# Optimization experiments

Measured on AMD Instinct MI355X. Metric: run time of the kernel, lower is better.

The kernel has to match this reference:

```python
import jax, jax.numpy as jnp
import numpy as np

B, C, T, V = 16, 128, 64, 512
H = 8
AC = C // H  # att_channel = 16
NEG = -1e9


def setup_inputs() -> dict:
    key = jax.random.key(0)
    ks = jax.random.split(key, 6)
    x = jax.random.normal(ks[0], (B, C, T, V), dtype=jnp.float32)
    # additive temporal mask: causal (upper triangle masked out)
    mask = jnp.where(jnp.triu(jnp.ones((T, T), dtype=bool), k=1), NEG, 0.0).astype(jnp.float32)
    # to_qkv: nn.Linear(att_channel -> 3*att_channel); torch weight is [out, in]
    w_qkv = jax.random.normal(ks[1], (3 * AC, AC), dtype=jnp.float32) / np.sqrt(AC)
    b_qkv = jax.random.normal(ks[2], (3 * AC,), dtype=jnp.float32) * 0.02
    # proj: Linear(n_channel -> n_channel)
    w_proj = jax.random.normal(ks[3], (C, C), dtype=jnp.float32) / np.sqrt(C)
    b_proj = jax.random.normal(ks[4], (C,), dtype=jnp.float32) * 0.02
    return {"x": x, "mask": mask, "w_qkv": w_qkv, "b_qkv": b_qkv,
            "w_proj": w_proj, "b_proj": b_proj}


def reference(x, mask, w_qkv, b_qkv, w_proj, b_proj):
    # split_head: 'b (h c) t v -> (b h) v t c'
    xh = x.reshape(B, H, AC, T, V)
    xh = jnp.transpose(xh, (0, 1, 4, 3, 2)).reshape(B * H, V, T, AC)
    # to_qkv on last dim
    qkv = jnp.einsum('nvtc,oc->nvto', xh, w_qkv) + b_qkv
    q, k, v = qkv[..., :AC], qkv[..., AC:2 * AC], qkv[..., 2 * AC:]
    # attention over time, batched over (b h, v)
    att = jnp.einsum('nvtc,nvsc->nvts', q, k) / jnp.sqrt(jnp.float32(AC)) + mask
    att = jax.nn.softmax(att, axis=-1)
    out = jnp.einsum('nvts,nvsc->nvtc', att, v)  # [(b h), v, t, c]
    # concat_head: '(b h) v t c -> b (h c) t v'
    out = out.reshape(B, H, V, T, AC)
    out = jnp.transpose(out, (0, 1, 4, 3, 2)).reshape(B, C, T, V)
    # proj: bctv -> bvtc, Linear(C->C), back
    y = jnp.einsum('bctv,oc->botv', out, w_proj) + b_proj[None, :, None, None]
    return y
```

## Files before the change

### kernel.cpp

```cpp
#include <hip/hip_runtime.h>
#include <math.h>

#define B_ 16
#define C_ 128
#define T_ 64
#define V_ 512
#define H_ 8

typedef short shortx8 __attribute__((ext_vector_type(8)));
typedef float floatx16 __attribute__((ext_vector_type(16)));

static __device__ __forceinline__ unsigned int f2bf(float f) {
  unsigned int u = __float_as_uint(f);
  return (u + 0x7FFFu + ((u >> 16) & 1u)) >> 16;
}


__global__ __launch_bounds__(256) void precompute_kernel(
    const float* __restrict__ w_qkv,
    const float* __restrict__ b_qkv,
    const float* __restrict__ w_proj,
    const float* __restrict__ b_proj,
    float* __restrict__ ws) {
  const float SC = 0.25f * 1.4426950408889634f;
  int tid = threadIdx.x;

  {
    int c = tid >> 4, cp = tid & 15;
    float s = 0.f;
    for (int a = 0; a < 16; ++a)
      s += w_qkv[a * 16 + c] * w_qkv[(16 + a) * 16 + cp];
    ws[c * 16 + cp] = s * SC;
  }
  if (tid < 16) {
    float s = 0.f;
    for (int a = 0; a < 16; ++a)
      s += b_qkv[a] * w_qkv[(16 + a) * 16 + tid];
    ws[256 + tid] = s * SC;
  }
  if (tid < 128) {
    float s = b_proj[tid];
    for (int a = 0; a < 16; ++a) {
      float wpsum = 0.f;
      for (int h = 0; h < 8; ++h) wpsum += w_proj[tid * 128 + h * 16 + a];
      s += wpsum * b_qkv[32 + a];
    }
    ws[272 + tid] = s;
  }
  unsigned short* gf = (unsigned short*)(ws + 512);
  for (int k = 0; k < 64; ++k) {
    int idx = tid + 256 * k;
    int o = idx >> 7;
    int hc = idx & 127;
    int h = hc >> 4, c = hc & 15;
    float s = 0.f;
    for (int a = 0; a < 16; ++a)
      s += w_proj[o * 128 + h * 16 + a] * w_qkv[(32 + a) * 16 + c];
    int w = o >> 5, lm = o & 31;
    int kk = hc >> 4;
    int half = (hc >> 3) & 1;
    int j = hc & 7;
    int lane = half * 32 + lm;
    gf[((w * 8 + kk) * 64 + lane) * 8 + j] = (unsigned short)f2bf(s);
  }
}

__global__ __launch_bounds__(256, 2) void attn_kernel(
    const float* __restrict__ x,
    const float* __restrict__ ws,
    float* __restrict__ out) {
  __shared__ float Xs[16][64][16];

  int blk = blockIdx.x;
  int vt = blk & 31;
  int h  = (blk >> 5) & 7;
  int b  = blk >> 8;
  int v0 = vt * 16;
  int tid = threadIdx.x;

  const float* xb = x + ((size_t)(b * C_ + h * 16) * T_) * V_ + v0;
  #pragma unroll
  for (int k = 0; k < 16; ++k) {
    int i4 = tid + 256 * k;
    int vq = (i4 & 3) * 4;
    int s  = (i4 >> 2) & 63;
    int c  = i4 >> 8;
    *(float4*)&Xs[c][s][vq] = *(const float4*)(xb + ((size_t)c * 64 + s) * 512 + vq);
  }
  __syncthreads();

  const float* M = ws;
  const float* u = ws + 256;
  int vl = tid & 15;
  int tq = tid >> 4;
  int t0 = tq * 4;

  float q2[4][16];
  #pragma unroll
  for (int cp = 0; cp < 16; ++cp) {
    float uv = u[cp];
    q2[0][cp] = uv; q2[1][cp] = uv; q2[2][cp] = uv; q2[3][cp] = uv;
  }
  #pragma unroll
  for (int c = 0; c < 16; ++c) {
    float x0 = Xs[c][t0 + 0][vl];
    float x1 = Xs[c][t0 + 1][vl];
    float x2 = Xs[c][t0 + 2][vl];
    float x3 = Xs[c][t0 + 3][vl];
    #pragma unroll
    for (int cp = 0; cp < 16; ++cp) {
      float m = M[c * 16 + cp];
      q2[0][cp] += x0 * m; q2[1][cp] += x1 * m;
      q2[2][cp] += x2 * m; q2[3][cp] += x3 * m;
    }
  }

  float z[4][16];
  #pragma unroll
  for (int tt = 0; tt < 4; ++tt)
    #pragma unroll
    for (int c = 0; c < 16; ++c) z[tt][c] = 0.f;
  float sum0 = 0.f, sum1 = 0.f, sum2 = 0.f, sum3 = 0.f;

  for (int s = 0; s <= t0 + 3; ++s) {
    float xr[16];
    #pragma unroll
    for (int c = 0; c < 16; ++c) xr[c] = Xs[c][s][vl];
    float d0 = 0.f, d1 = 0.f, d2 = 0.f, d3 = 0.f;
    #pragma unroll
    for (int c = 0; c < 16; ++c) {
      d0 += q2[0][c] * xr[c];
      d1 += q2[1][c] * xr[c];
      d2 += q2[2][c] * xr[c];
      d3 += q2[3][c] * xr[c];
    }
    float e0 = (s <= t0 + 0) ? __builtin_amdgcn_exp2f(d0) : 0.f;
    float e1 = (s <= t0 + 1) ? __builtin_amdgcn_exp2f(d1) : 0.f;
    float e2 = (s <= t0 + 2) ? __builtin_amdgcn_exp2f(d2) : 0.f;
    float e3 = __builtin_amdgcn_exp2f(d3);
    sum0 += e0; sum1 += e1; sum2 += e2; sum3 += e3;
    #pragma unroll
    for (int c = 0; c < 16; ++c) {
      z[0][c] += e0 * xr[c];
      z[1][c] += e1 * xr[c];
      z[2][c] += e2 * xr[c];
      z[3][c] += e3 * xr[c];
    }
  }

  float rsum[4] = {1.f / sum0, 1.f / sum1, 1.f / sum2, 1.f / sum3};

  #pragma unroll
  for (int tt = 0; tt < 4; ++tt) {
    float rs = rsum[tt];
    int t = t0 + tt;
    size_t PB = (size_t)b * (C_ * T_ * V_) + (size_t)t * V_ + (size_t)(vt >> 2) * 64;
    #pragma unroll
    for (int half = 0; half < 2; ++half) {
      int hcblk = 2 * h + half;
      uint4 pk;
      unsigned int* pw = (unsigned int*)&pk;
      #pragma unroll
      for (int wq = 0; wq < 4; ++wq) {
        int c = half * 8 + wq * 2;
        pw[wq] = f2bf(z[tt][c] * rs) | (f2bf(z[tt][c + 1] * rs) << 16);
      }
      float* dst = out + PB + (size_t)(hcblk * 4 + (vt & 3)) * (T_ * V_) + vl * 4;
      *(uint4*)dst = pk;
    }
  }
}

__global__ __launch_bounds__(256) void proj_kernel(
    const float* __restrict__ ws,
    float* __restrict__ out) {
  int blk = blockIdx.x;
  int vt = blk & 7;
  int t  = (blk >> 3) & 63;
  int b  = blk >> 9;
  int v0 = vt * 64;
  int tid = threadIdx.x;
  int l  = tid & 63;
  int w  = tid >> 6;
  int lh = l >> 5;
  int lm = l & 31;

  size_t PB = (size_t)b * (C_ * T_ * V_) + (size_t)t * V_ + v0;

  const short* gf = (const short*)(ws + 512);
  shortx8 g[8];
  #pragma unroll
  for (int kk = 0; kk < 8; ++kk)
    g[kk] = *(const shortx8*)(gf + (size_t)((w * 8 + kk) * 64 + l) * 8);

  shortx8 bz0[8], bz1[8];
  #pragma unroll
  for (int kk = 0; kk < 8; ++kk) {
    int hcblk = 2 * kk + lh;
    {
      int tvl = lm;
      bz0[kk] = *(const shortx8*)(out + PB + (size_t)(hcblk * 4 + (tvl >> 4)) * 32768 + (tvl & 15) * 4);
    }
    {
      int tvl = 32 + lm;
      bz1[kk] = *(const shortx8*)(out + PB + (size_t)(hcblk * 4 + (tvl >> 4)) * 32768 + (tvl & 15) * 4);
    }
  }

  float yb[16];
  const float* ybp = ws + 272;
  #pragma unroll
  for (int r = 0; r < 16; ++r) {
    int row = (r & 3) + 8 * (r >> 2) + 4 * lh;
    yb[r] = ybp[32 * w + row];
  }

  asm volatile("s_waitcnt vmcnt(0)" ::: "memory");
  __syncthreads();

  floatx16 acc0, acc1;
  #pragma unroll
  for (int i = 0; i < 16; ++i) { acc0[i] = 0.f; acc1[i] = 0.f; }

  #pragma unroll
  for (int kk = 0; kk < 8; ++kk) {
    acc0 = __builtin_amdgcn_mfma_f32_32x32x16_bf16(g[kk], bz0[kk], acc0, 0, 0, 0);
    acc1 = __builtin_amdgcn_mfma_f32_32x32x16_bf16(g[kk], bz1[kk], acc1, 0, 0, 0);
  }

  #pragma unroll
  for (int r = 0; r < 16; ++r) {
    int row = (r & 3) + 8 * (r >> 2) + 4 * lh;
    size_t off = PB + (size_t)(32 * w + row) * 32768;
    out[off + lm]      = acc0[r] + yb[r];
    out[off + 32 + lm] = acc1[r] + yb[r];
  }
}

extern "C" void kernel_launch(void* const* d_in, const int* in_sizes, int n_in,
                              void* d_out, int out_size, void* d_ws, size_t ws_size,
                              hipStream_t stream) {
  const float* x      = (const float*)d_in[0];
  const float* w_qkv  = (const float*)d_in[2];
  const float* b_qkv  = (const float*)d_in[3];
  const float* w_proj = (const float*)d_in[4];
  const float* b_proj = (const float*)d_in[5];
  float* out = (float*)d_out;
  float* ws  = (float*)d_ws;

  hipLaunchKernelGGL(precompute_kernel, dim3(1), dim3(256), 0, stream,
                     w_qkv, b_qkv, w_proj, b_proj, ws);
  hipLaunchKernelGGL(attn_kernel, dim3(4096), dim3(256), 0, stream, x, ws, out);
  hipLaunchKernelGGL(proj_kernel, dim3(8192), dim3(256), 0, stream, ws, out);
}
```

Measured before the change: 691.1 us.

## Move attention inner products to fp16 MFMA with fp16 LDS staging

Measured after the change: 596.5 us. -13.7%, faster.

```diff
diff --git a/kernel.cpp b/kernel.cpp
--- a/kernel.cpp
+++ b/kernel.cpp
@@ -6,15 +6,29 @@
 #define T_ 64
 #define V_ 512
 #define H_ 8
-
-typedef short shortx8 __attribute__((ext_vector_type(8)));
-typedef float floatx16 __attribute__((ext_vector_type(16)));
-
-static __device__ __forceinline__ unsigned int f2bf(float f) {
-  unsigned int u = __float_as_uint(f);
-  return (u + 0x7FFFu + ((u >> 16) & 1u)) >> 16;
-}
-
+#define TV_ 32768
+#define CTV_ 4194304
+
+typedef __fp16 fp16x2 __attribute__((ext_vector_type(2)));
+typedef _Float16 f16x4 __attribute__((ext_vector_type(4)));
+typedef _Float16 f16x8 __attribute__((ext_vector_type(8)));
+typedef float f32x4 __attribute__((ext_vector_type(4)));
+typedef float f32x16 __attribute__((ext_vector_type(16)));
+
+union U4 { f16x4 v; fp16x2 h2[2]; unsigned int u[2]; };
+
+static __device__ __forceinline__ f16x4 pk4(float a, float b, float c, float d) {
+  U4 r;
+  r.h2[0] = __builtin_amdgcn_cvt_pkrtz(a, b);
+  r.h2[1] = __builtin_amdgcn_cvt_pkrtz(c, d);
+  return r.v;
+}
+
+static __device__ __forceinline__ unsigned short f2h(float f) {
+  union { _Float16 h; unsigned short u; } c;
+  c.h = (_Float16)f;
+  return c.u;
+}
 
 __global__ __launch_bounds__(256) void precompute_kernel(
     const float* __restrict__ w_qkv,
@@ -61,15 +75,15 @@
     int half = (hc >> 3) & 1;
     int j = hc & 7;
     int lane = half * 32 + lm;
-    gf[((w * 8 + kk) * 64 + lane) * 8 + j] = (unsigned short)f2bf(s);
-  }
-}
-
-__global__ __launch_bounds__(256, 2) void attn_kernel(
+    gf[((w * 8 + kk) * 64 + lane) * 8 + j] = f2h(s);
+  }
+}
+
+__global__ __launch_bounds__(256, 4) void attn_kernel(
     const float* __restrict__ x,
     const float* __restrict__ ws,
     float* __restrict__ out) {
-  __shared__ float Xs[16][64][16];
+  __shared__ unsigned short Xh[16 * 1024];
 
   int blk = blockIdx.x;
   int vt = blk & 31;
@@ -77,96 +91,99 @@
   int b  = blk >> 8;
   int v0 = vt * 16;
   int tid = threadIdx.x;
-
-  const float* xb = x + ((size_t)(b * C_ + h * 16) * T_) * V_ + v0;
-  #pragma unroll
-  for (int k = 0; k < 16; ++k) {
-    int i4 = tid + 256 * k;
-    int vq = (i4 & 3) * 4;
-    int s  = (i4 >> 2) & 63;
-    int c  = i4 >> 8;
-    *(float4*)&Xs[c][s][vq] = *(const float4*)(xb + ((size_t)c * 64 + s) * 512 + vq);
+  int l  = tid & 63;
+  int wv = tid >> 6;
+  int m  = l & 15;
+  int g  = l >> 4;
+
+  const float* Mw = ws;
+  const float* uw = ws + 256;
+  f16x4 Mf = pk4(Mw[(4 * g + 0) * 16 + m], Mw[(4 * g + 1) * 16 + m],
+                 Mw[(4 * g + 2) * 16 + m], Mw[(4 * g + 3) * 16 + m]);
+  f32x4 uin = { uw[4 * g + 0], uw[4 * g + 1], uw[4 * g + 2], uw[4 * g + 3] };
+
+  {
+    int vq = (tid & 3) * 4;
+    int ts = (tid >> 2) & 15;
+    int cxor = (tid & 3) << 1;
+    const float* xb = x + ((size_t)(b * C_ + h * 16) * T_) * V_ + v0;
+    #pragma unroll 4
+    for (int it = 0; it < 16; ++it) {
+      int c = wv * 4 + (it & 3);
+      int t = ts + 16 * (it >> 2);
+      float4 f = *(const float4*)(xb + ((size_t)c * 64 + t) * 512 + vq);
+      int base = t * 16 + (c ^ cxor);
+      Xh[(vq + 0) * 1024 + base] = f2h(f.x);
+      Xh[(vq + 1) * 1024 + base] = f2h(f.y);
+      Xh[(vq + 2) * 1024 + base] = f2h(f.z);
+      Xh[(vq + 3) * 1024 + base] = f2h(f.w);
+    }
   }
   __syncthreads();
 
-  const float* M = ws;
-  const float* u = ws + 256;
-  int vl = tid & 15;
-  int tq = tid >> 4;
-  int t0 = tq * 4;
-
-  float q2[4][16];
-  #pragma unroll
-  for (int cp = 0; cp < 16; ++cp) {
-    float uv = u[cp];
-    q2[0][cp] = uv; q2[1][cp] = uv; q2[2][cp] = uv; q2[3][cp] = uv;
-  }
-  #pragma unroll
-  for (int c = 0; c < 16; ++c) {
-    float x0 = Xs[c][t0 + 0][vl];
-    float x1 = Xs[c][t0 + 1][vl];
-    float x2 = Xs[c][t0 + 2][vl];
-    float x3 = Xs[c][t0 + 3][vl];
+  size_t obase = (size_t)b * CTV_ + (size_t)(8 * h + (vt & 3)) * TV_ + (vt >> 2) * 64;
+  f32x4 zc = {0.f, 0.f, 0.f, 0.f};
+
+  #pragma unroll 1
+  for (int i = 0; i < 4; ++i) {
+    int vloc = 4 * i + wv;
+    const unsigned short* xv = Xh + (vloc << 10);
+
+    f16x4 XF[4];
     #pragma unroll
-    for (int cp = 0; cp < 16; ++cp) {
-      float m = M[c * 16 + cp];
-      q2[0][cp] += x0 * m; q2[1][cp] += x1 * m;
-      q2[2][cp] += x2 * m; q2[3][cp] += x3 * m;
-    }
-  }
-
-  float z[4][16];
-  #pragma unroll
-  for (int tt = 0; tt < 4; ++tt)
+    for (int ti = 0; ti < 4; ++ti) {
+      U4 xf;
+      xf.v = *(const f16x4*)(xv + 256 * ti + 16 * m + 4 * (g ^ (i >> 1)));
+      if (i & 1) { unsigned tw = xf.u[0]; xf.u[0] = xf.u[1]; xf.u[1] = tw; }
+      XF[ti] = xf.v;
+    }
+    f16x4 XC[4];
+    {
+      const unsigned short* xc = xv + (m ^ (2 * i)) + 64 * g;
+      #pragma unroll
+      for (int si = 0; si < 4; ++si) {
+        const unsigned short* p = xc + 256 * si;
+        U4 t4;
+        t4.u[0] = (unsigned)p[0]  | ((unsigned)p[16] << 16);
+        t4.u[1] = (unsigned)p[32] | ((unsigned)p[48] << 16);
+        XC[si] = t4.v;
+      }
+    }
+
     #pragma unroll
-    for (int c = 0; c < 16; ++c) z[tt][c] = 0.f;
-  float sum0 = 0.f, sum1 = 0.f, sum2 = 0.f, sum3 = 0.f;
-
-  for (int s = 0; s <= t0 + 3; ++s) {
-    float xr[16];
-    #pragma unroll
-    for (int c = 0; c < 16; ++c) xr[c] = Xs[c][s][vl];
-    float d0 = 0.f, d1 = 0.f, d2 = 0.f, d3 = 0.f;
-    #pragma unroll
-    for (int c = 0; c < 16; ++c) {
-      d0 += q2[0][c] * xr[c];
-      d1 += q2[1][c] * xr[c];
-      d2 += q2[2][c] * xr[c];
-      d3 += q2[3][c] * xr[c];
-    }
-    float e0 = (s <= t0 + 0) ? __builtin_amdgcn_exp2f(d0) : 0.f;
-    float e1 = (s <= t0 + 1) ? __builtin_amdgcn_exp2f(d1) : 0.f;
-    float e2 = (s <= t0 + 2) ? __builtin_amdgcn_exp2f(d2) : 0.f;
-    float e3 = __builtin_amdgcn_exp2f(d3);
-    sum0 += e0; sum1 += e1; sum2 += e2; sum3 += e3;
-    #pragma unroll
-    for (int c = 0; c < 16; ++c) {
-      z[0][c] += e0 * xr[c];
-      z[1][c] += e1 * xr[c];
-      z[2][c] += e2 * xr[c];
-      z[3][c] += e3 * xr[c];
-    }
-  }
-
-  float rsum[4] = {1.f / sum0, 1.f / sum1, 1.f / sum2, 1.f / sum3};
-
-  #pragma unroll
-  for (int tt = 0; tt < 4; ++tt) {
-    float rs = rsum[tt];
-    int t = t0 + tt;
-    size_t PB = (size_t)b * (C_ * T_ * V_) + (size_t)t * V_ + (size_t)(vt >> 2) * 64;
-    #pragma unroll
-    for (int half = 0; half < 2; ++half) {
-      int hcblk = 2 * h + half;
-      uint4 pk;
-      unsigned int* pw = (unsigned int*)&pk;
+    for (int ti = 0; ti < 4; ++ti) {
+      f32x4 q2 = __builtin_amdgcn_mfma_f32_16x16x16f16(Mf, XF[ti], uin, 0, 0, 0);
+      f16x4 q2f = pk4(q2[0], q2[1], q2[2], q2[3]);
+      f32x4 z = zc;
+      float ps = 0.f;
       #pragma unroll
-      for (int wq = 0; wq < 4; ++wq) {
-        int c = half * 8 + wq * 2;
-        pw[wq] = f2bf(z[tt][c] * rs) | (f2bf(z[tt][c + 1] * rs) << 16);
+      for (int si = 0; si <= ti; ++si) {
+        f32x4 s4 = __builtin_amdgcn_mfma_f32_16x16x16f16(XF[si], q2f, zc, 0, 0, 0);
+        float e0 = __builtin_amdgcn_exp2f(s4[0]);
+        float e1 = __builtin_amdgcn_exp2f(s4[1]);
+        float e2 = __builtin_amdgcn_exp2f(s4[2]);
+        float e3 = __builtin_amdgcn_exp2f(s4[3]);
+        if (si == ti) {
+          e0 = (4 * g + 0 <= m) ? e0 : 0.f;
+          e1 = (4 * g + 1 <= m) ? e1 : 0.f;
+          e2 = (4 * g + 2 <= m) ? e2 : 0.f;
+          e3 = (4 * g + 3 <= m) ? e3 : 0.f;
+        }
+        ps += (e0 + e1) + (e2 + e3);
+        f16x4 pf = pk4(e0, e1, e2, e3);
+        z = __builtin_amdgcn_mfma_f32_16x16x16f16(XC[si], pf, z, 0, 0, 0);
       }
-      float* dst = out + PB + (size_t)(hcblk * 4 + (vt & 3)) * (T_ * V_) + vl * 4;
-      *(uint4*)dst = pk;
+      ps += __shfl_xor(ps, 16);
+      ps += __shfl_xor(ps, 32);
+      float rs = 1.f / ps;
+      U4 zz;
+      zz.h2[0] = __builtin_amdgcn_cvt_pkrtz(z[0] * rs, z[1] * rs);
+      zz.h2[1] = __builtin_amdgcn_cvt_pkrtz(z[2] * rs, z[3] * rs);
+      int t = 16 * ti + m;
+      float* dst = out + obase + (size_t)((g >> 1) * 4) * TV_ + (size_t)t * V_
+                   + vloc * 4 + ((2 * g) & 3);
+      uint2 st; st.x = zz.u[0]; st.y = zz.u[1];
+      *(uint2*)dst = st;
     }
   }
 }
@@ -185,25 +202,25 @@
   int lh = l >> 5;
   int lm = l & 31;
 
-  size_t PB = (size_t)b * (C_ * T_ * V_) + (size_t)t * V_ + v0;
-
-  const short* gf = (const short*)(ws + 512);
-  shortx8 g[8];
+  size_t PB = (size_t)b * CTV_ + (size_t)t * V_ + v0;
+
+  const unsigned short* gfp = (const unsigned short*)(ws + 512);
+  f16x8 gfr[8];
   #pragma unroll
   for (int kk = 0; kk < 8; ++kk)
-    g[kk] = *(const shortx8*)(gf + (size_t)((w * 8 + kk) * 64 + l) * 8);
-
-  shortx8 bz0[8], bz1[8];
+    gfr[kk] = *(const f16x8*)(gfp + (size_t)((w * 8 + kk) * 64 + l) * 8);
+
+  f16x8 bz0[8], bz1[8];
   #pragma unroll
   for (int kk = 0; kk < 8; ++kk) {
     int hcblk = 2 * kk + lh;
     {
       int tvl = lm;
-      bz0[kk] = *(const shortx8*)(out + PB + (size_t)(hcblk * 4 + (tvl >> 4)) * 32768 + (tvl & 15) * 4);
+      bz0[kk] = *(const f16x8*)(out + PB + (size_t)(hcblk * 4 + (tvl >> 4)) * TV_ + (tvl & 15) * 4);
     }
     {
       int tvl = 32 + lm;
-      bz1[kk] = *(const shortx8*)(out + PB + (size_t)(hcblk * 4 + (tvl >> 4)) * 32768 + (tvl & 15) * 4);
+      bz1[kk] = *(const f16x8*)(out + PB + (size_t)(hcblk * 4 + (tvl >> 4)) * TV_ + (tvl & 15) * 4);
     }
   }
 
@@ -218,20 +235,20 @@
   asm volatile("s_waitcnt vmcnt(0)" ::: "memory");
   __syncthreads();
 
-  floatx16 acc0, acc1;
+  f32x16 acc0, acc1;
   #pragma unroll
   for (int i = 0; i < 16; ++i) { acc0[i] = 0.f; acc1[i] = 0.f; }
 
   #pragma unroll
   for (int kk = 0; kk < 8; ++kk) {
-    acc0 = __builtin_amdgcn_mfma_f32_32x32x16_bf16(g[kk], bz0[kk], acc0, 0, 0, 0);
-    acc1 = __builtin_amdgcn_mfma_f32_32x32x16_bf16(g[kk], bz1[kk], acc1, 0, 0, 0);
+    acc0 = __builtin_amdgcn_mfma_f32_32x32x16_f16(gfr[kk], bz0[kk], acc0, 0, 0, 0);
+    acc1 = __builtin_amdgcn_mfma_f32_32x32x16_f16(gfr[kk], bz1[kk], acc1, 0, 0, 0);
   }
 
   #pragma unroll
   for (int r = 0; r < 16; ++r) {
     int row = (r & 3) + 8 * (r >> 2) + 4 * lh;
-    size_t off = PB + (size_t)(32 * w + row) * 32768;
+    size_t off = PB + (size_t)(32 * w + row) * TV_;
     out[off + lm]      = acc0[r] + yb[r];
     out[off + 32 + lm] = acc1[r] + yb[r];
   }
```
